# Performance work log

Measured on AMD Instinct MI355X. Metric: run time of the kernel, lower is better.

Reference implementation:

```python
import jax, jax.numpy as jnp
import numpy as np

N = 4_194_304   # batch
DIM = 2         # dim
K = 5           # n_potentials
EPS = 1.0       # epsilon
S_INIT = 0.1    # S_diagonal_init


def setup_inputs() -> dict:
    key = jax.random.key(0)
    k1, k2, k3, k4 = jax.random.split(key, 4)
    x = jax.random.normal(k1, (N, DIM), dtype=jnp.float32)
    r = jax.random.normal(k2, (K, DIM), dtype=jnp.float32)
    log_S = jnp.log(S_INIT * jnp.ones((K, DIM), dtype=jnp.float32))
    log_alpha = jnp.log(jnp.ones(K, dtype=jnp.float32) / K)
    # pre-drawn randomness for the mixture sample (one categorical + one normal per row)
    gumbel = jax.random.gumbel(k3, (N, K), dtype=jnp.float32)
    noise = jax.random.normal(k4, (N, DIM), dtype=jnp.float32)
    return {"x": x, "r": r, "log_S": log_S, "log_alpha": log_alpha,
            "gumbel": gumbel, "noise": noise}


def reference(x, r, log_S, log_alpha, gumbel, noise):
    # Fused equivalent of LightSBplus.forward: per-row diagonal-Gaussian
    S = jnp.exp(log_S)                                   # [K, D]
    logits = ((x * x) @ S.T + 2.0 * (x @ r.T)) / (2.0 * EPS) + log_alpha  # [N, K]
    idx = jnp.argmax(logits + gumbel, axis=-1)           # categorical sample, [N]
    Sk = S[idx]                                          # [N, D]
    rk = r[idx]                                          # [N, D]
    mean = rk + Sk * x                                   # r_k + S_k * x
    return mean + jnp.sqrt(EPS * Sk) * noise
```

## Files before the change

### kernel.cpp

```cpp
#include <hip/hip_runtime.h>
#include <math.h>

#define KPOT 5
#define THREADS 256
#define ROWS_PER_BLOCK 1024

#define XFLOATS (ROWS_PER_BLOCK * 2)
#define GFLOATS (ROWS_PER_BLOCK * KPOT)

__device__ __forceinline__ void load_lds16(const float* gptr, float* lptr) {
    __builtin_amdgcn_global_load_lds(
        (const __attribute__((address_space(1))) void*)gptr,
        (__attribute__((address_space(3))) void*)lptr, 16, 0, 0);
}

__global__ __launch_bounds__(THREADS) void lightsb_kernel(
    const float* __restrict__ x,
    const float* __restrict__ r,
    const float* __restrict__ log_S,
    const float* __restrict__ log_alpha,
    const float* __restrict__ gumbel,
    const float* __restrict__ noise,
    float* __restrict__ out,
    int n_rows)
{
    __shared__ float xsh[XFLOATS];
    __shared__ float nsh[XFLOATS];
    __shared__ float gsh[GFLOATS];

    const int t = threadIdx.x;
    const long long blockRow0 = (long long)blockIdx.x * ROWS_PER_BLOCK;

    float S0[KPOT], S1[KPOT], r0[KPOT], r1[KPOT], la[KPOT], q0[KPOT], q1[KPOT];

    if (blockRow0 + ROWS_PER_BLOCK <= n_rows) {
        const int w    = t >> 6;
        const int lane = t & 63;

        const float* xg = x      + blockRow0 * 2;
        const float* ng = noise  + blockRow0 * 2;
        const float* gg = gumbel + blockRow0 * KPOT;

#pragma unroll
        for (int j = 0; j < 2; ++j) {
            const int c = w + 4 * j;
            load_lds16(xg + c * 256 + lane * 4, &xsh[c * 256]);
            load_lds16(ng + c * 256 + lane * 4, &nsh[c * 256]);
        }
#pragma unroll
        for (int j = 0; j < 5; ++j) {
            const int c = w + 4 * j;
            load_lds16(gg + c * 256 + lane * 4, &gsh[c * 256]);
        }

#pragma unroll
        for (int k = 0; k < KPOT; ++k) {
            float s0 = expf(log_S[2 * k + 0]);
            float s1 = expf(log_S[2 * k + 1]);
            S0[k] = s0;  S1[k] = s1;
            r0[k] = r[2 * k + 0];  r1[k] = r[2 * k + 1];
            la[k] = log_alpha[k];
            q0[k] = sqrtf(s0);  q1[k] = sqrtf(s1);
        }

        __syncthreads();

        const float4* xs4 = reinterpret_cast<const float4*>(xsh);
        const float4* ns4 = reinterpret_cast<const float4*>(nsh);
        float4* o4 = reinterpret_cast<float4*>(out) + blockRow0 / 2;

#pragma unroll
        for (int p = 0; p < 2; ++p) {
            const float4 xv = xs4[p * 256 + t];
            const float4 nv = ns4[p * 256 + t];
            const int lr0 = p * 512 + 2 * t;
            const float* g0 = &gsh[lr0 * KPOT];
            float ov[4];

#pragma unroll
            for (int h = 0; h < 2; ++h) {
                const float xx0 = (h == 0) ? xv.x : xv.z;
                const float xx1 = (h == 0) ? xv.y : xv.w;
                const float nn0 = (h == 0) ? nv.x : nv.z;
                const float nn1 = (h == 0) ? nv.y : nv.w;
                const float* g = g0 + h * KPOT;

                const float u0 = 0.5f * xx0 * xx0;
                const float u1 = 0.5f * xx1 * xx1;

                float best = fmaf(S0[0], u0, fmaf(S1[0], u1,
                             fmaf(r0[0], xx0, fmaf(r1[0], xx1, la[0] + g[0]))));
                float bS0 = S0[0], bS1 = S1[0];
                float br0 = r0[0], br1 = r1[0];
                float bq0 = q0[0], bq1 = q1[0];
#pragma unroll
                for (int k = 1; k < KPOT; ++k) {
                    float s = fmaf(S0[k], u0, fmaf(S1[k], u1,
                              fmaf(r0[k], xx0, fmaf(r1[k], xx1, la[k] + g[k]))));
                    bool c = s > best;
                    best = c ? s : best;
                    bS0 = c ? S0[k] : bS0;
                    bS1 = c ? S1[k] : bS1;
                    br0 = c ? r0[k] : br0;
                    br1 = c ? r1[k] : br1;
                    bq0 = c ? q0[k] : bq0;
                    bq1 = c ? q1[k] : bq1;
                }
                ov[2 * h + 0] = fmaf(bS0, xx0, fmaf(bq0, nn0, br0));
                ov[2 * h + 1] = fmaf(bS1, xx1, fmaf(bq1, nn1, br1));
            }
            o4[p * 256 + t] = make_float4(ov[0], ov[1], ov[2], ov[3]);
        }
    } else {
#pragma unroll
        for (int k = 0; k < KPOT; ++k) {
            float s0 = expf(log_S[2 * k + 0]);
            float s1 = expf(log_S[2 * k + 1]);
            S0[k] = s0;  S1[k] = s1;
            r0[k] = r[2 * k + 0];  r1[k] = r[2 * k + 1];
            la[k] = log_alpha[k];
            q0[k] = sqrtf(s0);  q1[k] = sqrtf(s1);
        }
        for (long long row = blockRow0 + t; row < n_rows; row += THREADS) {
            float x0 = x[row * 2 + 0];
            float x1 = x[row * 2 + 1];
            float u0 = 0.5f * x0 * x0;
            float u1 = 0.5f * x1 * x1;
            float best = fmaf(S0[0], u0, fmaf(S1[0], u1,
                         fmaf(r0[0], x0, fmaf(r1[0], x1, la[0] + gumbel[row * KPOT + 0]))));
            int bidx = 0;
#pragma unroll
            for (int k = 1; k < KPOT; ++k) {
                float s = fmaf(S0[k], u0, fmaf(S1[k], u1,
                          fmaf(r0[k], x0, fmaf(r1[k], x1, la[k] + gumbel[row * KPOT + k]))));
                if (s > best) { best = s; bidx = k; }
            }
            float n0 = noise[row * 2 + 0];
            float n1 = noise[row * 2 + 1];
            out[row * 2 + 0] = fmaf(S0[bidx], x0, fmaf(q0[bidx], n0, r0[bidx]));
            out[row * 2 + 1] = fmaf(S1[bidx], x1, fmaf(q1[bidx], n1, r1[bidx]));
        }
    }
}

extern "C" void kernel_launch(void* const* d_in, const int* in_sizes, int n_in,
                              void* d_out, int out_size, void* d_ws, size_t ws_size,
                              hipStream_t stream) {
    const float* x         = (const float*)d_in[0];
    const float* r         = (const float*)d_in[1];
    const float* log_S     = (const float*)d_in[2];
    const float* log_alpha = (const float*)d_in[3];
    const float* gumbel    = (const float*)d_in[4];
    const float* noise     = (const float*)d_in[5];
    float* out = (float*)d_out;

    const int n_rows = in_sizes[0] / 2;
    const int grid = (n_rows + ROWS_PER_BLOCK - 1) / ROWS_PER_BLOCK;

    lightsb_kernel<<<grid, THREADS, 0, stream>>>(x, r, log_S, log_alpha,
                                                 gumbel, noise, out, n_rows);
}
```

Before: 189.1 us.

## Convert to persistent grid with double-buffered LDS prefetch of tiles

Replaces the one-tile-per-block launch with a grid-stride persistent kernel capped at 512 blocks. Each block prefetches the next tile's x, noise and gumbel into a second LDS buffer through global_load_lds while it computes the current tile. The aim is to overlap the DMA loads with compute, cut block launch overhead, and compute the per-potential constants once per block instead of once per tile. It doubles LDS use per block, and the barrier at the end of each iteration may force waits on the in-flight prefetch, which would limit the overlap. Tail rows are handled by a separate grid-stride scalar loop.

```diff
diff --git a/kernel.cpp b/kernel.cpp
--- a/kernel.cpp
+++ b/kernel.cpp
@@ -3,10 +3,10 @@
 
 #define KPOT 5
 #define THREADS 256
-#define ROWS_PER_BLOCK 1024
-
-#define XFLOATS (ROWS_PER_BLOCK * 2)
-#define GFLOATS (ROWS_PER_BLOCK * KPOT)
+#define TROWS 1024
+#define XF (TROWS * 2)
+#define GF (TROWS * KPOT)
+#define NBLOCKS 512
 
 __device__ __forceinline__ void load_lds16(const float* gptr, float* lptr) {
     __builtin_amdgcn_global_load_lds(
@@ -24,57 +24,66 @@
     float* __restrict__ out,
     int n_rows)
 {
-    __shared__ float xsh[XFLOATS];
-    __shared__ float nsh[XFLOATS];
-    __shared__ float gsh[GFLOATS];
+    __shared__ float xsh[2][XF];
+    __shared__ float nsh[2][XF];
+    __shared__ float gsh[2][GF];
 
-    const int t = threadIdx.x;
-    const long long blockRow0 = (long long)blockIdx.x * ROWS_PER_BLOCK;
+    const int t    = threadIdx.x;
+    const int w    = t >> 6;
+    const int lane = t & 63;
+    const long long ntiles = n_rows / TROWS;
+    const long long stride = gridDim.x;
 
     float S0[KPOT], S1[KPOT], r0[KPOT], r1[KPOT], la[KPOT], q0[KPOT], q1[KPOT];
 
-    if (blockRow0 + ROWS_PER_BLOCK <= n_rows) {
-        const int w    = t >> 6;
-        const int lane = t & 63;
+#define STAGE(buf, tile)                                                        \
+    do {                                                                        \
+        const float* xg = x      + (tile) * (TROWS * 2);                        \
+        const float* ng = noise  + (tile) * (TROWS * 2);                        \
+        const float* gg = gumbel + (tile) * (TROWS * KPOT);                     \
+        _Pragma("unroll")                                                       \
+        for (int j = 0; j < 2; ++j) {                                           \
+            const int c = w + 4 * j;                                            \
+            load_lds16(xg + c * 256 + lane * 4, &xsh[buf][c * 256]);            \
+            load_lds16(ng + c * 256 + lane * 4, &nsh[buf][c * 256]);            \
+        }                                                                       \
+        _Pragma("unroll")                                                       \
+        for (int j = 0; j < 5; ++j) {                                           \
+            const int c = w + 4 * j;                                            \
+            load_lds16(gg + c * 256 + lane * 4, &gsh[buf][c * 256]);            \
+        }                                                                       \
+    } while (0)
 
-        const float* xg = x      + blockRow0 * 2;
-        const float* ng = noise  + blockRow0 * 2;
-        const float* gg = gumbel + blockRow0 * KPOT;
+    long long tile = blockIdx.x;
+    if (tile < ntiles) STAGE(0, tile);
 
 #pragma unroll
-        for (int j = 0; j < 2; ++j) {
-            const int c = w + 4 * j;
-            load_lds16(xg + c * 256 + lane * 4, &xsh[c * 256]);
-            load_lds16(ng + c * 256 + lane * 4, &nsh[c * 256]);
-        }
-#pragma unroll
-        for (int j = 0; j < 5; ++j) {
-            const int c = w + 4 * j;
-            load_lds16(gg + c * 256 + lane * 4, &gsh[c * 256]);
-        }
+    for (int k = 0; k < KPOT; ++k) {
+        float s0 = expf(log_S[2 * k + 0]);
+        float s1 = expf(log_S[2 * k + 1]);
+        S0[k] = s0;  S1[k] = s1;
+        r0[k] = r[2 * k + 0];  r1[k] = r[2 * k + 1];
+        la[k] = log_alpha[k];
+        q0[k] = sqrtf(s0);  q1[k] = sqrtf(s1);
+    }
 
-#pragma unroll
-        for (int k = 0; k < KPOT; ++k) {
-            float s0 = expf(log_S[2 * k + 0]);
-            float s1 = expf(log_S[2 * k + 1]);
-            S0[k] = s0;  S1[k] = s1;
-            r0[k] = r[2 * k + 0];  r1[k] = r[2 * k + 1];
-            la[k] = log_alpha[k];
-            q0[k] = sqrtf(s0);  q1[k] = sqrtf(s1);
-        }
+    __syncthreads();
 
-        __syncthreads();
+    int cur = 0;
+    for (; tile < ntiles; tile += stride) {
+        const long long nxt = tile + stride;
+        if (nxt < ntiles) STAGE(cur ^ 1, nxt);
 
-        const float4* xs4 = reinterpret_cast<const float4*>(xsh);
-        const float4* ns4 = reinterpret_cast<const float4*>(nsh);
-        float4* o4 = reinterpret_cast<float4*>(out) + blockRow0 / 2;
+        const float4* xs4 = reinterpret_cast<const float4*>(xsh[cur]);
+        const float4* ns4 = reinterpret_cast<const float4*>(nsh[cur]);
+        const float*  gs  = gsh[cur];
+        float4* o4 = reinterpret_cast<float4*>(out) + tile * (TROWS / 2);
 
 #pragma unroll
         for (int p = 0; p < 2; ++p) {
             const float4 xv = xs4[p * 256 + t];
             const float4 nv = ns4[p * 256 + t];
-            const int lr0 = p * 512 + 2 * t;
-            const float* g0 = &gsh[lr0 * KPOT];
+            const float* g0 = &gs[(p * 512 + 2 * t) * KPOT];
             float ov[4];
 
 #pragma unroll
@@ -111,36 +120,32 @@
             }
             o4[p * 256 + t] = make_float4(ov[0], ov[1], ov[2], ov[3]);
         }
-    } else {
+
+        __syncthreads();
+        cur ^= 1;
+    }
+
+    for (long long row = ntiles * TROWS + (long long)blockIdx.x * THREADS + t;
+         row < n_rows; row += stride * THREADS) {
+        float x0 = x[row * 2 + 0];
+        float x1 = x[row * 2 + 1];
+        float u0 = 0.5f * x0 * x0;
+        float u1 = 0.5f * x1 * x1;
+        float best = fmaf(S0[0], u0, fmaf(S1[0], u1,
+                     fmaf(r0[0], x0, fmaf(r1[0], x1, la[0] + gumbel[row * KPOT + 0]))));
+        int bidx = 0;
 #pragma unroll
-        for (int k = 0; k < KPOT; ++k) {
-            float s0 = expf(log_S[2 * k + 0]);
-            float s1 = expf(log_S[2 * k + 1]);
-            S0[k] = s0;  S1[k] = s1;
-            r0[k] = r[2 * k + 0];  r1[k] = r[2 * k + 1];
-            la[k] = log_alpha[k];
-            q0[k] = sqrtf(s0);  q1[k] = sqrtf(s1);
+        for (int k = 1; k < KPOT; ++k) {
+            float s = fmaf(S0[k], u0, fmaf(S1[k], u1,
+                      fmaf(r0[k], x0, fmaf(r1[k], x1, la[k] + gumbel[row * KPOT + k]))));
+            if (s > best) { best = s; bidx = k; }
         }
-        for (long long row = blockRow0 + t; row < n_rows; row += THREADS) {
-            float x0 = x[row * 2 + 0];
-            float x1 = x[row * 2 + 1];
-            float u0 = 0.5f * x0 * x0;
-            float u1 = 0.5f * x1 * x1;
-            float best = fmaf(S0[0], u0, fmaf(S1[0], u1,
-                         fmaf(r0[0], x0, fmaf(r1[0], x1, la[0] + gumbel[row * KPOT + 0]))));
-            int bidx = 0;
-#pragma unroll
-            for (int k = 1; k < KPOT; ++k) {
-                float s = fmaf(S0[k], u0, fmaf(S1[k], u1,
-                          fmaf(r0[k], x0, fmaf(r1[k], x1, la[k] + gumbel[row * KPOT + k]))));
-                if (s > best) { best = s; bidx = k; }
-            }
-            float n0 = noise[row * 2 + 0];
-            float n1 = noise[row * 2 + 1];
-            out[row * 2 + 0] = fmaf(S0[bidx], x0, fmaf(q0[bidx], n0, r0[bidx]));
-            out[row * 2 + 1] = fmaf(S1[bidx], x1, fmaf(q1[bidx], n1, r1[bidx]));
-        }
+        float n0 = noise[row * 2 + 0];
+        float n1 = noise[row * 2 + 1];
+        out[row * 2 + 0] = fmaf(S0[bidx], x0, fmaf(q0[bidx], n0, r0[bidx]));
+        out[row * 2 + 1] = fmaf(S1[bidx], x1, fmaf(q1[bidx], n1, r1[bidx]));
     }
+#undef STAGE
 }
 
 extern "C" void kernel_launch(void* const* d_in, const int* in_sizes, int n_in,
@@ -155,7 +160,8 @@
     float* out = (float*)d_out;
 
     const int n_rows = in_sizes[0] / 2;
-    const int grid = (n_rows + ROWS_PER_BLOCK - 1) / ROWS_PER_BLOCK;
+    const long long ntiles = n_rows / TROWS;
+    int grid = (int)((ntiles < NBLOCKS) ? (ntiles > 0 ? ntiles : 1) : NBLOCKS);
 
     lightsb_kernel<<<grid, THREADS, 0, stream>>>(x, r, log_S, log_alpha,
                                                  gumbel, noise, out, n_rows);
```

New measurement: 189.7 us. About the same (+0.3%).
